# Performance work log

Measured on AMD Instinct MI355X. Metric: run time of the kernel, lower is better.

The kernel has to match this reference:

```python
import jax, jax.numpy as jnp
import numpy as np
from jax import lax

C_IN = 256
C_OUT = 256
KS = 3


def _conv(x, w, b):
    # x: [B,C,H,W], w: [O,I,kh,kw] -> NCHW 'SAME' conv, stride 1
    y = lax.conv_general_dilated(x, w, window_strides=(1, 1), padding='SAME',
                                 dimension_numbers=('NCHW', 'OIHW', 'NCHW'))
    return y + b[None, :, None, None]


def setup_inputs() -> dict:
    key = jax.random.key(0)
    ks = jax.random.split(key, 7)
    B, H, W = 2, 64, 64
    fan = C_IN * KS * KS
    lim = float(np.sqrt(6.0 / (fan + C_OUT * KS * KS)))  # xavier uniform
    return {
        'x': jax.random.normal(ks[0], (B, C_IN, H, W), jnp.float32),
        'ref_x': jax.random.normal(ks[1], (B, C_IN, H, W), jnp.float32),
        'conv1_w': jax.random.uniform(ks[2], (C_OUT, C_IN, KS, KS), jnp.float32, -lim, lim),
        'conv1_b': jnp.zeros((C_OUT,), jnp.float32),
        'conv2_w': jax.random.uniform(ks[3], (C_OUT, C_IN, KS, KS), jnp.float32, -lim, lim),
        'conv2_b': jnp.zeros((C_OUT,), jnp.float32),
        'gamma': jnp.array([0.5], jnp.float32),
    }


def reference(x, ref_x, conv1_w, conv1_b, conv2_w, conv2_b, gamma):
    B, Cin, H, W = x.shape
    HW = H * W
    x_f = jax.nn.relu(_conv(x, conv1_w, conv1_b)).reshape(B, C_OUT, HW)        # [B,C,HW]
    r_f = jax.nn.relu(_conv(ref_x, conv1_w, conv1_b))                          # [B,C,H,W]
    r_f = r_f.transpose(0, 2, 3, 1).reshape(B, HW, C_OUT)                      # [B,HW,C]
    corr = jnp.einsum('bnc,bcm->bnm', r_f, x_f)                                # [B,HW,HW]
    corr = jax.nn.softmax(corr, axis=1)                                        # softmax over ref positions
    ref_c2 = jax.nn.relu(_conv(x, conv2_w, conv2_b)).reshape(B, C_OUT, HW)     # [B,C,HW]
    A = jnp.einsum('bcn,bnm->bcm', ref_c2, corr).reshape(x.shape)              # [B,C,H,W]
    return A * gamma[0] + x
```

## Files before the change

### kernel.cpp

```cpp
#include <hip/hip_runtime.h>
#include <hip/hip_bf16.h>

#define B_ 2
#define C_ 256
#define H_ 64
#define W_ 64
#define N_ 4096

typedef short bf16x8 __attribute__((ext_vector_type(8)));
typedef _Float16 f16x8 __attribute__((ext_vector_type(8)));
typedef float f32x4 __attribute__((ext_vector_type(4)));

static __device__ __forceinline__ unsigned short f2bf(float f) {
    union { float f; unsigned u; } uf; uf.f = f;
    unsigned r = uf.u + 0x7fffu + ((uf.u >> 16) & 1u);
    return (unsigned short)(r >> 16);
}
static __device__ __forceinline__ unsigned short f2h_u(float f) {
    union { _Float16 h; unsigned short u; } c; c.h = (_Float16)f; return c.u;
}

static __device__ __forceinline__ void gload16(const void* g, void* l) {
    __builtin_amdgcn_global_load_lds(
        (const __attribute__((address_space(1))) unsigned int*)g,
        (__attribute__((address_space(3))) unsigned int*)l, 16, 0, 0);
}

__global__ __launch_bounds__(256) void cvt_x_k(const float* __restrict__ x,
                                               const float* __restrict__ ref_x,
                                               unsigned short* __restrict__ xtx,
                                               unsigned short* __restrict__ xtr)
{
    __shared__ unsigned short t[64][72];
    const int pt = blockIdx.x, ct = blockIdx.y;
    const int which = blockIdx.z >> 1, b = blockIdx.z & 1;
    const float* in = which ? ref_x : x;
    unsigned short* out = which ? xtr : xtx;
    const int a = threadIdx.x & 63, r = threadIdx.x >> 6;
    #pragma unroll
    for (int i = 0; i < 16; ++i) {
        int c = i * 4 + r;
        t[c][a] = f2h_u(in[((size_t)(b * C_ + ct * 64 + c) << 12) + pt * 64 + a]);
    }
    __syncthreads();
    #pragma unroll
    for (int i = 0; i < 16; ++i) {
        int p = i * 4 + r;
        out[((size_t)(b * N_ + pt * 64 + p) << 8) + ct * 64 + a] = t[a][p];
    }
}

__global__ __launch_bounds__(256) void cvt_w_k(const float* __restrict__ w1,
                                               const float* __restrict__ w2,
                                               unsigned short* __restrict__ wh1,
                                               unsigned short* __restrict__ wh2)
{
    int g = blockIdx.x;
    const float* w = (g < 2304) ? w1 : w2;
    unsigned short* wh = (g < 2304) ? wh1 : wh2;
    int i = (g % 2304) * 256 + threadIdx.x;
    int ci = i & 255, co = (i >> 8) & 255, tap = i >> 16;
    wh[i] = f2h_u(w[((size_t)(co * 256 + ci)) * 9 + tap]);
}

__global__ __launch_bounds__(256) void conv_mfma_k(
    const unsigned short* __restrict__ xtx, const unsigned short* __restrict__ xtr,
    const unsigned short* __restrict__ w1h, const unsigned short* __restrict__ w2h,
    const float* __restrict__ b1, const float* __restrict__ b2,
    unsigned short* __restrict__ f1x, unsigned short* __restrict__ f1r,
    unsigned short* __restrict__ f2)
{
    __shared__ unsigned short As[4 * 576 * 8];
    __shared__ unsigned short Bs[4 * 66 * 32];
    const int tid = threadIdx.x;
    const int pt  = blockIdx.x;
    const int cot = blockIdx.y;
    const int cid = blockIdx.z >> 1;
    const int b   = blockIdx.z & 1;

    const unsigned short* xt = (cid == 1) ? xtr : xtx;
    const unsigned short* wt = (cid == 2) ? w2h : w1h;
    const float* bias = (cid == 2) ? b2 : b1;
    unsigned short* out = (cid == 0) ? f1x : (cid == 1) ? f1r : f2;
    const int trans = (cid != 2);

    const int lane = tid & 63, wid = tid >> 6;
    const int wco = wid >> 1, wpos = wid & 1;
    const int rl = lane & 15, q = lane >> 4;
    const int r0 = pt * 2;

    f32x4 acc[2][4];
    #pragma unroll
    for (int mi = 0; mi < 2; ++mi)
        #pragma unroll
        for (int ni = 0; ni < 4; ++ni)
            #pragma unroll
            for (int e = 0; e < 4; ++e) acc[mi][ni][e] = 0.f;

    for (int k0 = 0; k0 < C_; k0 += 32) {
        #pragma unroll
        for (int tap = 0; tap < 9; ++tap) {
            gload16(wt + ((size_t)(tap * C_ + cot * 64 + lane) << 8) + k0 + wid * 8,
                    &As[(wid * 576 + tap * 64 + lane) * 8]);
        }
        #pragma unroll
        for (int j = 0; j < 5; ++j) {
            int it = tid + j * 256;
            if (it < 1056) {
                int col = it >> 4, sub = it & 15;
                int row = sub >> 2, qb = sub & 3;
                int h = r0 + row - 1, c = col - 1;
                float4 v; v.x = 0.f; v.y = 0.f; v.z = 0.f; v.w = 0.f;
                if (h >= 0 && h < 64 && c >= 0 && c < 64)
                    v = *(const float4*)(xt + ((size_t)(b * N_ + h * 64 + c) << 8) + k0 + qb * 8);
                int chunk = qb ^ ((col >> 1) & 3);
                *(float4*)&Bs[(row * 66 + col) * 32 + chunk * 8] = v;
            }
        }
        __syncthreads();

        #pragma unroll
        for (int tap = 0; tap < 9; ++tap) {
            const int kh = tap / 3, kw = tap % 3;
            f16x8 a0 = *(const f16x8*)&As[(q * 576 + tap * 64 + wco * 32 + rl) * 8];
            f16x8 a1 = *(const f16x8*)&As[(q * 576 + tap * 64 + wco * 32 + 16 + rl) * 8];
            const int chunkB = q ^ (((rl + kw) >> 1) & 3);
            const int rowB = (wpos + kh) * 66;
            #pragma unroll
            for (int ni = 0; ni < 4; ++ni) {
                int colB = ni * 16 + rl + kw;
                f16x8 bf = *(const f16x8*)&Bs[(rowB + colB) * 32 + chunkB * 8];
                acc[0][ni] = __builtin_amdgcn_mfma_f32_16x16x32_f16(a0, bf, acc[0][ni], 0, 0, 0);
                acc[1][ni] = __builtin_amdgcn_mfma_f32_16x16x32_f16(a1, bf, acc[1][ni], 0, 0, 0);
            }
        }
        __syncthreads();
    }

    #pragma unroll
    for (int mi = 0; mi < 2; ++mi) {
        const int co = cot * 64 + wco * 32 + mi * 16 + q * 4;
        float bs[4];
        #pragma unroll
        for (int rr = 0; rr < 4; ++rr) bs[rr] = bias[co + rr];
        #pragma unroll
        for (int ni = 0; ni < 4; ++ni) {
            const int pos = pt * 128 + wpos * 64 + ni * 16 + rl;
            if (trans) {
                unsigned short pk[4];
                #pragma unroll
                for (int rr = 0; rr < 4; ++rr)
                    pk[rr] = f2bf(fmaxf(acc[mi][ni][rr] + bs[rr], 0.f));
                uint2 u;
                u.x = (unsigned)pk[0] | ((unsigned)pk[1] << 16);
                u.y = (unsigned)pk[2] | ((unsigned)pk[3] << 16);
                *(uint2*)&out[((size_t)(b * N_ + pos) << 8) + co] = u;
            } else {
                #pragma unroll
                for (int rr = 0; rr < 4; ++rr)
                    out[((size_t)(b * C_ + co + rr) << 12) + pos] =
                        f2bf(fmaxf(acc[mi][ni][rr] + bs[rr], 0.f));
            }
        }
    }
}

__global__ __launch_bounds__(256) void gemm_corr_k(
    const unsigned short* __restrict__ f1x, const unsigned short* __restrict__ f1r,
    float* __restrict__ corr)
{
    __shared__ alignas(16) unsigned short As[128 * 32];
    __shared__ alignas(16) unsigned short Bs[128 * 32];
    const int tid = threadIdx.x;
    const int tn = blockIdx.x, tm = blockIdx.y, b = blockIdx.z;

    const unsigned short* Ab = f1x + ((size_t)b * N_ + (size_t)tm * 128) * C_;
    const unsigned short* Bb = f1r + ((size_t)b * N_ + (size_t)tn * 128) * C_;

    const int wid = tid >> 6, lane = tid & 63;
    const int wr = wid >> 1, wc = wid & 1;
    const int rl = lane & 15, q = lane >> 4;
    const int srow = wid * 32 + (lane >> 2), sq = lane & 3;

    f32x4 acc[4][4];
    #pragma unroll
    for (int mi = 0; mi < 4; ++mi)
        #pragma unroll
        for (int ni = 0; ni < 4; ++ni)
            #pragma unroll
            for (int e = 0; e < 4; ++e) acc[mi][ni][e] = 0.f;

    for (int k0 = 0; k0 < C_; k0 += 32) {
        gload16(&Ab[(size_t)srow * C_ + k0 + sq * 8],        &As[srow * 32 + sq * 8]);
        gload16(&Ab[(size_t)(srow + 16) * C_ + k0 + sq * 8], &As[(srow + 16) * 32 + sq * 8]);
        gload16(&Bb[(size_t)srow * C_ + k0 + sq * 8],        &Bs[srow * 32 + sq * 8]);
        gload16(&Bb[(size_t)(srow + 16) * C_ + k0 + sq * 8], &Bs[(srow + 16) * 32 + sq * 8]);
        __syncthreads();
        bf16x8 a[4], bb[4];
        #pragma unroll
        for (int mi = 0; mi < 4; ++mi)
            a[mi] = *(const bf16x8*)&As[(wr * 64 + mi * 16 + rl) * 32 + q * 8];
        #pragma unroll
        for (int ni = 0; ni < 4; ++ni)
            bb[ni] = *(const bf16x8*)&Bs[(wc * 64 + ni * 16 + rl) * 32 + q * 8];
        #pragma unroll
        for (int mi = 0; mi < 4; ++mi)
            #pragma unroll
            for (int ni = 0; ni < 4; ++ni)
                acc[mi][ni] = __builtin_amdgcn_mfma_f32_16x16x32_bf16(a[mi], bb[ni], acc[mi][ni], 0, 0, 0);
        __syncthreads();
    }

    #pragma unroll
    for (int mi = 0; mi < 4; ++mi)
        #pragma unroll
        for (int ni = 0; ni < 4; ++ni)
            #pragma unroll
            for (int rr = 0; rr < 4; ++rr) {
                int m = tm * 128 + wr * 64 + mi * 16 + q * 4 + rr;
                int n = tn * 128 + wc * 64 + ni * 16 + rl;
                corr[((size_t)b * N_ + m) * N_ + n] = acc[mi][ni][rr];
            }
}

__global__ __launch_bounds__(256) void softmax_rows_k(float* __restrict__ corr)
{
    __shared__ float red[4];
    const int m = blockIdx.x, b = blockIdx.y;
    float* row = corr + ((size_t)b * N_ + m) * N_;
    float4* row4 = (float4*)row;
    const int tid = threadIdx.x;
    const int wid = tid >> 6, lane = tid & 63;

    float4 v[4];
    float mx = -3.0e38f;
    #pragma unroll
    for (int j = 0; j < 4; ++j) {
        v[j] = row4[tid + j * 256];
        mx = fmaxf(mx, fmaxf(fmaxf(v[j].x, v[j].y), fmaxf(v[j].z, v[j].w)));
    }
    #pragma unroll
    for (int off = 32; off; off >>= 1) mx = fmaxf(mx, __shfl_xor(mx, off));
    if (lane == 0) red[wid] = mx;
    __syncthreads();
    mx = fmaxf(fmaxf(red[0], red[1]), fmaxf(red[2], red[3]));
    __syncthreads();

    float s = 0.f;
    #pragma unroll
    for (int j = 0; j < 4; ++j) {
        v[j].x = __expf(v[j].x - mx);
        v[j].y = __expf(v[j].y - mx);
        v[j].z = __expf(v[j].z - mx);
        v[j].w = __expf(v[j].w - mx);
        s += v[j].x + v[j].y + v[j].z + v[j].w;
    }
    #pragma unroll
    for (int off = 32; off; off >>= 1) s += __shfl_xor(s, off);
    if (lane == 0) red[wid] = s;
    __syncthreads();
    s = red[0] + red[1] + red[2] + red[3];
    const float inv = 1.f / s;

    unsigned short* rb = (unsigned short*)row;
    #pragma unroll
    for (int j = 0; j < 4; ++j) {
        uint2 u;
        u.x = (unsigned)f2bf(v[j].x * inv) | ((unsigned)f2bf(v[j].y * inv) << 16);
        u.y = (unsigned)f2bf(v[j].z * inv) | ((unsigned)f2bf(v[j].w * inv) << 16);
        *(uint2*)&rb[4 * (tid + j * 256)] = u;
    }
}

__global__ __launch_bounds__(512) void gemm_out_k(
    const unsigned short* __restrict__ f2, float* __restrict__ corr)
{
    __shared__ alignas(16) unsigned short As[128 * 32];
    __shared__ alignas(16) unsigned short Bs[128 * 32];
    const int tid = threadIdx.x;
    const int tm = blockIdx.x;
    const int tc = blockIdx.y >> 2;
    const int s  = blockIdx.y & 3;
    const int b  = blockIdx.z;

    const unsigned short* Ab = f2 + ((size_t)b * C_ + (size_t)tc * 128) * N_;
    const unsigned short* Bb = (const unsigned short*)corr
                             + ((size_t)b * N_ + (size_t)tm * 128) * 8192;

    const int wid = tid >> 6, lane = tid & 63;
    const int wc = wid >> 2, wm = wid & 3;
    const int rl = lane & 15, q = lane >> 4;
    const int srow = wid * 16 + (lane >> 2), sq = lane & 3;
    const int nbase = s * 1024;

    f32x4 acc[4][2];
    #pragma unroll
    for (int mi = 0; mi < 4; ++mi)
        #pragma unroll
        for (int ni = 0; ni < 2; ++ni)
            #pragma unroll
            for (int e = 0; e < 4; ++e) acc[mi][ni][e] = 0.f;

    for (int kk = 0; kk < 32; ++kk) {
        const int k0 = nbase + kk * 32;
        gload16(&Ab[(size_t)srow * N_ + k0 + sq * 8],   &As[srow * 32 + sq * 8]);
        gload16(&Bb[(size_t)srow * 8192 + k0 + sq * 8], &Bs[srow * 32 + sq * 8]);
        __syncthreads();
        bf16x8 a[4], bb[2];
        #pragma unroll
        for (int mi = 0; mi < 4; ++mi)
            a[mi] = *(const bf16x8*)&As[(wc * 64 + mi * 16 + rl) * 32 + q * 8];
        #pragma unroll
        for (int ni = 0; ni < 2; ++ni)
            bb[ni] = *(const bf16x8*)&Bs[(wm * 32 + ni * 16 + rl) * 32 + q * 8];
        #pragma unroll
        for (int mi = 0; mi < 4; ++mi)
            #pragma unroll
            for (int ni = 0; ni < 2; ++ni)
                acc[mi][ni] = __builtin_amdgcn_mfma_f32_16x16x32_bf16(a[mi], bb[ni], acc[mi][ni], 0, 0, 0);
        __syncthreads();
    }

    #pragma unroll
    for (int mi = 0; mi < 4; ++mi)
        #pragma unroll
        for (int ni = 0; ni < 2; ++ni)
            #pragma unroll
            for (int rr = 0; rr < 4; ++rr) {
                int c = tc * 128 + wc * 64 + mi * 16 + q * 4 + rr;
                int m = tm * 128 + wm * 32 + ni * 16 + rl;
                size_t e = (((size_t)(s * 2 + b) * C_ + c) << 12) + m;
                corr[(e >> 11) * 4096 + 2048 + (e & 2047)] = acc[mi][ni][rr];
            }
}

__global__ __launch_bounds__(256) void reduce_k(
    const float* __restrict__ corr, const float* __restrict__ x,
    const float* __restrict__ gamma, float* __restrict__ out)
{
    const float g = gamma[0];
    size_t i = (size_t)blockIdx.x * 256 + threadIdx.x;
    size_t idx = i << 2;
    float4 sum; sum.x = 0.f; sum.y = 0.f; sum.z = 0.f; sum.w = 0.f;
    #pragma unroll
    for (int sp = 0; sp < 4; ++sp) {
        size_t e = (size_t)sp * 2097152 + idx;
        float4 v = *(const float4*)&corr[(e >> 11) * 4096 + 2048 + (e & 2047)];
        sum.x += v.x; sum.y += v.y; sum.z += v.z; sum.w += v.w;
    }
    float4 xv = ((const float4*)x)[i];
    float4 o;
    o.x = sum.x * g + xv.x;
    o.y = sum.y * g + xv.y;
    o.z = sum.z * g + xv.z;
    o.w = sum.w * g + xv.w;
    ((float4*)out)[i] = o;
}

extern "C" void kernel_launch(void* const* d_in, const int* in_sizes, int n_in,
                              void* d_out, int out_size, void* d_ws, size_t ws_size,
                              hipStream_t stream) {
    const float* x     = (const float*)d_in[0];
    const float* ref_x = (const float*)d_in[1];
    const float* w1    = (const float*)d_in[2];
    const float* b1    = (const float*)d_in[3];
    const float* w2    = (const float*)d_in[4];
    const float* b2    = (const float*)d_in[5];
    const float* gamma = (const float*)d_in[6];
    float* out = (float*)d_out;

    char* ws = (char*)d_ws;
    size_t off = 0;
    auto nxt = [&](size_t bytes) {
        char* p = ws + off;
        off += (bytes + 255) & ~(size_t)255;
        return p;
    };
    unsigned short* f1x = (unsigned short*)nxt((size_t)B_ * N_ * C_ * 2);
    unsigned short* f1r = (unsigned short*)nxt((size_t)B_ * N_ * C_ * 2);
    unsigned short* f2  = (unsigned short*)nxt((size_t)B_ * N_ * C_ * 2);
    unsigned short* xtx = (unsigned short*)nxt((size_t)B_ * N_ * C_ * 2);
    unsigned short* xtr = (unsigned short*)nxt((size_t)B_ * N_ * C_ * 2);
    unsigned short* w1h = (unsigned short*)nxt((size_t)9 * C_ * C_ * 2);
    unsigned short* w2h = (unsigned short*)nxt((size_t)9 * C_ * C_ * 2);
    float* corr = (float*)nxt((size_t)B_ * N_ * N_ * 4);

    cvt_x_k<<<dim3(64, 4, 4), 256, 0, stream>>>(x, ref_x, xtx, xtr);
    cvt_w_k<<<4608, 256, 0, stream>>>(w1, w2, w1h, w2h);

    conv_mfma_k<<<dim3(32, 4, 6), 256, 0, stream>>>(xtx, xtr, w1h, w2h, b1, b2,
                                                    f1x, f1r, f2);

    gemm_corr_k<<<dim3(32, 32, B_), 256, 0, stream>>>(f1x, f1r, corr);
    softmax_rows_k<<<dim3(N_, B_), 256, 0, stream>>>(corr);
    gemm_out_k<<<dim3(32, 8, B_), 512, 0, stream>>>(f2, corr);
    reduce_k<<<2048, 256, 0, stream>>>(corr, x, gamma, out);
}
```

Measured before the change: 162.3 us.

## Switch conv and correlation GEMMs to 32x32x16 MFMA with larger conv tiles

```diff
diff --git a/kernel.cpp b/kernel.cpp
--- a/kernel.cpp
+++ b/kernel.cpp
@@ -10,6 +10,7 @@
 typedef short bf16x8 __attribute__((ext_vector_type(8)));
 typedef _Float16 f16x8 __attribute__((ext_vector_type(8)));
 typedef float f32x4 __attribute__((ext_vector_type(4)));
+typedef float f32x16 __attribute__((ext_vector_type(16)));
 
 static __device__ __forceinline__ unsigned short f2bf(float f) {
     union { float f; unsigned u; } uf; uf.f = f;
@@ -70,8 +71,8 @@
     unsigned short* __restrict__ f1x, unsigned short* __restrict__ f1r,
     unsigned short* __restrict__ f2)
 {
-    __shared__ unsigned short As[4 * 576 * 8];
-    __shared__ unsigned short Bs[4 * 66 * 32];
+    __shared__ unsigned short As[9 * 64 * 32];
+    __shared__ unsigned short Bs[6 * 66 * 32];
     const int tid = threadIdx.x;
     const int pt  = blockIdx.x;
     const int cot = blockIdx.y;
@@ -85,30 +86,31 @@
     const int trans = (cid != 2);
 
     const int lane = tid & 63, wid = tid >> 6;
-    const int wco = wid >> 1, wpos = wid & 1;
-    const int rl = lane & 15, q = lane >> 4;
-    const int r0 = pt * 2;
-
-    f32x4 acc[2][4];
-    #pragma unroll
-    for (int mi = 0; mi < 2; ++mi)
-        #pragma unroll
-        for (int ni = 0; ni < 4; ++ni)
-            #pragma unroll
-            for (int e = 0; e < 4; ++e) acc[mi][ni][e] = 0.f;
+    const int rl32 = lane & 31, l5 = lane >> 5;
+    const int r0 = pt * 4;
+
+    f32x16 acc[2][2];
+    #pragma unroll
+    for (int fm = 0; fm < 2; ++fm)
+        #pragma unroll
+        for (int fn = 0; fn < 2; ++fn)
+            #pragma unroll
+            for (int e = 0; e < 16; ++e) acc[fm][fn][e] = 0.f;
 
     for (int k0 = 0; k0 < C_; k0 += 32) {
         #pragma unroll
         for (int tap = 0; tap < 9; ++tap) {
-            gload16(wt + ((size_t)(tap * C_ + cot * 64 + lane) << 8) + k0 + wid * 8,
-                    &As[(wid * 576 + tap * 64 + lane) * 8]);
+            gload16(wt + ((size_t)(tap * C_ + cot * 64 + wid * 16 + (lane >> 2)) << 8)
+                       + k0 + (lane & 3) * 8,
+                    &As[tap * 2048 + wid * 512 + lane * 8]);
         }
         #pragma unroll
-        for (int j = 0; j < 5; ++j) {
+        for (int j = 0; j < 7; ++j) {
             int it = tid + j * 256;
-            if (it < 1056) {
-                int col = it >> 4, sub = it & 15;
-                int row = sub >> 2, qb = sub & 3;
+            if (it < 1584) {
+                int col = it / 24;
+                int rem = it - col * 24;
+                int row = rem >> 2, qb = rem & 3;
                 int h = r0 + row - 1, c = col - 1;
                 float4 v; v.x = 0.f; v.y = 0.f; v.z = 0.f; v.w = 0.f;
                 if (h >= 0 && h < 64 && c >= 0 && c < 64)
@@ -122,47 +124,60 @@
         #pragma unroll
         for (int tap = 0; tap < 9; ++tap) {
             const int kh = tap / 3, kw = tap % 3;
-            f16x8 a0 = *(const f16x8*)&As[(q * 576 + tap * 64 + wco * 32 + rl) * 8];
-            f16x8 a1 = *(const f16x8*)&As[(q * 576 + tap * 64 + wco * 32 + 16 + rl) * 8];
-            const int chunkB = q ^ (((rl + kw) >> 1) & 3);
-            const int rowB = (wpos + kh) * 66;
-            #pragma unroll
-            for (int ni = 0; ni < 4; ++ni) {
-                int colB = ni * 16 + rl + kw;
-                f16x8 bf = *(const f16x8*)&Bs[(rowB + colB) * 32 + chunkB * 8];
-                acc[0][ni] = __builtin_amdgcn_mfma_f32_16x16x32_f16(a0, bf, acc[0][ni], 0, 0, 0);
-                acc[1][ni] = __builtin_amdgcn_mfma_f32_16x16x32_f16(a1, bf, acc[1][ni], 0, 0, 0);
+            f16x8 a[2][2], bb[2][2];
+            #pragma unroll
+            for (int fm = 0; fm < 2; ++fm)
+                #pragma unroll
+                for (int kk = 0; kk < 2; ++kk)
+                    a[fm][kk] = *(const f16x8*)&As[(tap * 64 + fm * 32 + rl32) * 32 + kk * 16 + l5 * 8];
+            #pragma unroll
+            for (int fn = 0; fn < 2; ++fn) {
+                const int colB = fn * 32 + rl32 + kw;
+                const int sw = ((rl32 + kw) >> 1) & 3;
+                #pragma unroll
+                for (int kk = 0; kk < 2; ++kk) {
+                    const int kc = kk * 2 + l5;
+                    bb[fn][kk] = *(const f16x8*)&Bs[((wid + kh) * 66 + colB) * 32 + (kc ^ sw) * 8];
+                }
+            }
+            #pragma unroll
+            for (int fm = 0; fm < 2; ++fm)
+                #pragma unroll
+                for (int fn = 0; fn < 2; ++fn)
+                    #pragma unroll
+                    for (int kk = 0; kk < 2; ++kk)
+                        acc[fm][fn] = __builtin_amdgcn_mfma_f32_32x32x16_f16(
+                            a[fm][kk], bb[fn][kk], acc[fm][fn], 0, 0, 0);
+        }
+        __syncthreads();
+    }
+
+    const int prow = r0 + wid;
+    #pragma unroll
+    for (int fm = 0; fm < 2; ++fm)
+        #pragma unroll
+        for (int fn = 0; fn < 2; ++fn) {
+            const int pos = prow * 64 + fn * 32 + rl32;
+            #pragma unroll
+            for (int g = 0; g < 4; ++g) {
+                const int co0 = cot * 64 + fm * 32 + g * 8 + l5 * 4;
+                if (trans) {
+                    unsigned short pk[4];
+                    #pragma unroll
+                    for (int rr = 0; rr < 4; ++rr)
+                        pk[rr] = f2bf(fmaxf(acc[fm][fn][g * 4 + rr] + bias[co0 + rr], 0.f));
+                    uint2 u;
+                    u.x = (unsigned)pk[0] | ((unsigned)pk[1] << 16);
+                    u.y = (unsigned)pk[2] | ((unsigned)pk[3] << 16);
+                    *(uint2*)&out[((size_t)(b * N_ + pos) << 8) + co0] = u;
+                } else {
+                    #pragma unroll
+                    for (int rr = 0; rr < 4; ++rr)
+                        out[((size_t)(b * C_ + co0 + rr) << 12) + pos] =
+                            f2bf(fmaxf(acc[fm][fn][g * 4 + rr] + bias[co0 + rr], 0.f));
+                }
             }
         }
-        __syncthreads();
-    }
-
-    #pragma unroll
-    for (int mi = 0; mi < 2; ++mi) {
-        const int co = cot * 64 + wco * 32 + mi * 16 + q * 4;
-        float bs[4];
-        #pragma unroll
-        for (int rr = 0; rr < 4; ++rr) bs[rr] = bias[co + rr];
-        #pragma unroll
-        for (int ni = 0; ni < 4; ++ni) {
-            const int pos = pt * 128 + wpos * 64 + ni * 16 + rl;
-            if (trans) {
-                unsigned short pk[4];
-                #pragma unroll
-                for (int rr = 0; rr < 4; ++rr)
-                    pk[rr] = f2bf(fmaxf(acc[mi][ni][rr] + bs[rr], 0.f));
-                uint2 u;
-                u.x = (unsigned)pk[0] | ((unsigned)pk[1] << 16);
-                u.y = (unsigned)pk[2] | ((unsigned)pk[3] << 16);
-                *(uint2*)&out[((size_t)(b * N_ + pos) << 8) + co] = u;
-            } else {
-                #pragma unroll
-                for (int rr = 0; rr < 4; ++rr)
-                    out[((size_t)(b * C_ + co + rr) << 12) + pos] =
-                        f2bf(fmaxf(acc[mi][ni][rr] + bs[rr], 0.f));
-            }
-        }
-    }
 }
 
 __global__ __launch_bounds__(256) void gemm_corr_k(
@@ -179,16 +194,16 @@
 
     const int wid = tid >> 6, lane = tid & 63;
     const int wr = wid >> 1, wc = wid & 1;
-    const int rl = lane & 15, q = lane >> 4;
+    const int rl32 = lane & 31, l5 = lane >> 5;
     const int srow = wid * 32 + (lane >> 2), sq = lane & 3;
 
-    f32x4 acc[4][4];
-    #pragma unroll
-    for (int mi = 0; mi < 4; ++mi)
-        #pragma unroll
-        for (int ni = 0; ni < 4; ++ni)
-            #pragma unroll
-            for (int e = 0; e < 4; ++e) acc[mi][ni][e] = 0.f;
+    f32x16 acc[2][2];
+    #pragma unroll
+    for (int fm = 0; fm < 2; ++fm)
+        #pragma unroll
+        for (int fn = 0; fn < 2; ++fn)
+            #pragma unroll
+            for (int e = 0; e < 16; ++e) acc[fm][fn][e] = 0.f;
 
     for (int k0 = 0; k0 < C_; k0 += 32) {
         gload16(&Ab[(size_t)srow * C_ + k0 + sq * 8],        &As[srow * 32 + sq * 8]);
@@ -196,31 +211,41 @@
         gload16(&Bb[(size_t)srow * C_ + k0 + sq * 8],        &Bs[srow * 32 + sq * 8]);
         gload16(&Bb[(size_t)(srow + 16) * C_ + k0 + sq * 8], &Bs[(srow + 16) * 32 + sq * 8]);
         __syncthreads();
-        bf16x8 a[4], bb[4];
-        #pragma unroll
-        for (int mi = 0; mi < 4; ++mi)
-            a[mi] = *(const bf16x8*)&As[(wr * 64 + mi * 16 + rl) * 32 + q * 8];
-        #pragma unroll
-        for (int ni = 0; ni < 4; ++ni)
-            bb[ni] = *(const bf16x8*)&Bs[(wc * 64 + ni * 16 + rl) * 32 + q * 8];
-        #pragma unroll
-        for (int mi = 0; mi < 4; ++mi)
-            #pragma unroll
-            for (int ni = 0; ni < 4; ++ni)
-                acc[mi][ni] = __builtin_amdgcn_mfma_f32_16x16x32_bf16(a[mi], bb[ni], acc[mi][ni], 0, 0, 0);
-        __syncthreads();
-    }
-
-    #pragma unroll
-    for (int mi = 0; mi < 4; ++mi)
-        #pragma unroll
-        for (int ni = 0; ni < 4; ++ni)
-            #pragma unroll
-            for (int rr = 0; rr < 4; ++rr) {
-                int m = tm * 128 + wr * 64 + mi * 16 + q * 4 + rr;
-                int n = tn * 128 + wc * 64 + ni * 16 + rl;
-                corr[((size_t)b * N_ + m) * N_ + n] = acc[mi][ni][rr];
+        bf16x8 a[2][2], bb[2][2];
+        #pragma unroll
+        for (int fm = 0; fm < 2; ++fm)
+            #pragma unroll
+            for (int kk = 0; kk < 2; ++kk)
+                a[fm][kk] = *(const bf16x8*)&As[(wr * 64 + fm * 32 + rl32) * 32 + kk * 16 + l5 * 8];
+        #pragma unroll
+        for (int fn = 0; fn < 2; ++fn)
+            #pragma unroll
+            for (int kk = 0; kk < 2; ++kk)
+                bb[fn][kk] = *(const bf16x8*)&Bs[(wc * 64 + fn * 32 + rl32) * 32 + kk * 16 + l5 * 8];
+        #pragma unroll
+        for (int fm = 0; fm < 2; ++fm)
+            #pragma unroll
+            for (int fn = 0; fn < 2; ++fn)
+                #pragma unroll
+                for (int kk = 0; kk < 2; ++kk)
+                    acc[fm][fn] = __builtin_amdgcn_mfma_f32_32x32x16_bf16(
+                        a[fm][kk], bb[fn][kk], acc[fm][fn], 0, 0, 0);
+        __syncthreads();
+    }
+
+    #pragma unroll
+    for (int fm = 0; fm < 2; ++fm)
+        #pragma unroll
+        for (int fn = 0; fn < 2; ++fn) {
+            const int n = tn * 128 + wc * 64 + fn * 32 + rl32;
+            #pragma unroll
+            for (int g = 0; g < 4; ++g) {
+                const int m0 = tm * 128 + wr * 64 + fm * 32 + g * 8 + l5 * 4;
+                #pragma unroll
+                for (int rr = 0; rr < 4; ++rr)
+                    corr[((size_t)b * N_ + m0 + rr) * N_ + n] = acc[fm][fn][g * 4 + rr];
             }
+        }
 }
 
 __global__ __launch_bounds__(256) void softmax_rows_k(float* __restrict__ corr)
@@ -388,7 +413,7 @@
     cvt_x_k<<<dim3(64, 4, 4), 256, 0, stream>>>(x, ref_x, xtx, xtr);
     cvt_w_k<<<4608, 256, 0, stream>>>(w1, w2, w1h, w2h);
 
-    conv_mfma_k<<<dim3(32, 4, 6), 256, 0, stream>>>(xtx, xtr, w1h, w2h, b1, b2,
+    conv_mfma_k<<<dim3(16, 4, 6), 256, 0, stream>>>(xtx, xtr, w1h, w2h, b1, b2,
                                                     f1x, f1r, f2);
 
     gemm_corr_k<<<dim3(32, 32, B_), 256, 0, stream>>>(f1x, f1r, corr);
```

Result: no change. 163.6 us (+0.8%).

## Restructure conv to 2-wave blocks with direct weight loads; swizzle GEMM LDS tiles

Applied to the files above, without the earlier changes.

```diff
diff --git a/kernel.cpp b/kernel.cpp
--- a/kernel.cpp
+++ b/kernel.cpp
@@ -63,14 +63,13 @@
     wh[i] = f2h_u(w[((size_t)(co * 256 + ci)) * 9 + tap]);
 }
 
-__global__ __launch_bounds__(256) void conv_mfma_k(
+__global__ __launch_bounds__(128) void conv_mfma_k(
     const unsigned short* __restrict__ xtx, const unsigned short* __restrict__ xtr,
     const unsigned short* __restrict__ w1h, const unsigned short* __restrict__ w2h,
     const float* __restrict__ b1, const float* __restrict__ b2,
     unsigned short* __restrict__ f1x, unsigned short* __restrict__ f1r,
     unsigned short* __restrict__ f2)
 {
-    __shared__ unsigned short As[4 * 576 * 8];
     __shared__ unsigned short Bs[4 * 66 * 32];
     const int tid = threadIdx.x;
     const int pt  = blockIdx.x;
@@ -85,27 +84,21 @@
     const int trans = (cid != 2);
 
     const int lane = tid & 63, wid = tid >> 6;
-    const int wco = wid >> 1, wpos = wid & 1;
     const int rl = lane & 15, q = lane >> 4;
     const int r0 = pt * 2;
 
-    f32x4 acc[2][4];
-    #pragma unroll
-    for (int mi = 0; mi < 2; ++mi)
-        #pragma unroll
-        for (int ni = 0; ni < 4; ++ni)
-            #pragma unroll
-            for (int e = 0; e < 4; ++e) acc[mi][ni][e] = 0.f;
+    f32x4 acc[4][4];
+    #pragma unroll
+    for (int cf = 0; cf < 4; ++cf)
+        #pragma unroll
+        for (int pf = 0; pf < 4; ++pf)
+            #pragma unroll
+            for (int e = 0; e < 4; ++e) acc[cf][pf][e] = 0.f;
 
     for (int k0 = 0; k0 < C_; k0 += 32) {
         #pragma unroll
-        for (int tap = 0; tap < 9; ++tap) {
-            gload16(wt + ((size_t)(tap * C_ + cot * 64 + lane) << 8) + k0 + wid * 8,
-                    &As[(wid * 576 + tap * 64 + lane) * 8]);
-        }
-        #pragma unroll
-        for (int j = 0; j < 5; ++j) {
-            int it = tid + j * 256;
+        for (int j = 0; j < 9; ++j) {
+            int it = tid + j * 128;
             if (it < 1056) {
                 int col = it >> 4, sub = it & 15;
                 int row = sub >> 2, qb = sub & 3;
@@ -122,44 +115,49 @@
         #pragma unroll
         for (int tap = 0; tap < 9; ++tap) {
             const int kh = tap / 3, kw = tap % 3;
-            f16x8 a0 = *(const f16x8*)&As[(q * 576 + tap * 64 + wco * 32 + rl) * 8];
-            f16x8 a1 = *(const f16x8*)&As[(q * 576 + tap * 64 + wco * 32 + 16 + rl) * 8];
-            const int chunkB = q ^ (((rl + kw) >> 1) & 3);
-            const int rowB = (wpos + kh) * 66;
-            #pragma unroll
-            for (int ni = 0; ni < 4; ++ni) {
-                int colB = ni * 16 + rl + kw;
-                f16x8 bf = *(const f16x8*)&Bs[(rowB + colB) * 32 + chunkB * 8];
-                acc[0][ni] = __builtin_amdgcn_mfma_f32_16x16x32_f16(a0, bf, acc[0][ni], 0, 0, 0);
-                acc[1][ni] = __builtin_amdgcn_mfma_f32_16x16x32_f16(a1, bf, acc[1][ni], 0, 0, 0);
+            f16x8 w[4];
+            #pragma unroll
+            for (int cf = 0; cf < 4; ++cf)
+                w[cf] = *(const f16x8*)&wt[((size_t)(tap * C_ + cot * 64 + cf * 16 + rl) << 8)
+                                           + k0 + q * 8];
+            const int rowB = (wid + kh) * 66;
+            const int swz = ((rl + kw) >> 1) & 3;
+            #pragma unroll
+            for (int pf = 0; pf < 4; ++pf) {
+                const int colB = pf * 16 + rl + kw;
+                f16x8 xv = *(const f16x8*)&Bs[(rowB + colB) * 32 + (q ^ swz) * 8];
+                #pragma unroll
+                for (int cf = 0; cf < 4; ++cf)
+                    acc[cf][pf] = __builtin_amdgcn_mfma_f32_16x16x32_f16(w[cf], xv, acc[cf][pf], 0, 0, 0);
             }
         }
         __syncthreads();
     }
 
-    #pragma unroll
-    for (int mi = 0; mi < 2; ++mi) {
-        const int co = cot * 64 + wco * 32 + mi * 16 + q * 4;
+    const int prow = r0 + wid;
+    #pragma unroll
+    for (int cf = 0; cf < 4; ++cf) {
+        const int co0 = cot * 64 + cf * 16 + q * 4;
         float bs[4];
         #pragma unroll
-        for (int rr = 0; rr < 4; ++rr) bs[rr] = bias[co + rr];
-        #pragma unroll
-        for (int ni = 0; ni < 4; ++ni) {
-            const int pos = pt * 128 + wpos * 64 + ni * 16 + rl;
+        for (int rr = 0; rr < 4; ++rr) bs[rr] = bias[co0 + rr];
+        #pragma unroll
+        for (int pf = 0; pf < 4; ++pf) {
+            const int pos = prow * 64 + pf * 16 + rl;
             if (trans) {
                 unsigned short pk[4];
                 #pragma unroll
                 for (int rr = 0; rr < 4; ++rr)
-                    pk[rr] = f2bf(fmaxf(acc[mi][ni][rr] + bs[rr], 0.f));
+                    pk[rr] = f2bf(fmaxf(acc[cf][pf][rr] + bs[rr], 0.f));
                 uint2 u;
                 u.x = (unsigned)pk[0] | ((unsigned)pk[1] << 16);
                 u.y = (unsigned)pk[2] | ((unsigned)pk[3] << 16);
-                *(uint2*)&out[((size_t)(b * N_ + pos) << 8) + co] = u;
+                *(uint2*)&out[((size_t)(b * N_ + pos) << 8) + co0] = u;
             } else {
                 #pragma unroll
                 for (int rr = 0; rr < 4; ++rr)
-                    out[((size_t)(b * C_ + co + rr) << 12) + pos] =
-                        f2bf(fmaxf(acc[mi][ni][rr] + bs[rr], 0.f));
+                    out[((size_t)(b * C_ + co0 + rr) << 12) + pos] =
+                        f2bf(fmaxf(acc[cf][pf][rr] + bs[rr], 0.f));
             }
         }
     }
@@ -181,6 +179,8 @@
     const int wr = wid >> 1, wc = wid & 1;
     const int rl = lane & 15, q = lane >> 4;
     const int srow = wid * 32 + (lane >> 2), sq = lane & 3;
+    const int logq = sq ^ ((lane >> 3) & 3);
+    const int rswz = (rl >> 1) & 3;
 
     f32x4 acc[4][4];
     #pragma unroll
@@ -191,18 +191,18 @@
             for (int e = 0; e < 4; ++e) acc[mi][ni][e] = 0.f;
 
     for (int k0 = 0; k0 < C_; k0 += 32) {
-        gload16(&Ab[(size_t)srow * C_ + k0 + sq * 8],        &As[srow * 32 + sq * 8]);
-        gload16(&Ab[(size_t)(srow + 16) * C_ + k0 + sq * 8], &As[(srow + 16) * 32 + sq * 8]);
-        gload16(&Bb[(size_t)srow * C_ + k0 + sq * 8],        &Bs[srow * 32 + sq * 8]);
-        gload16(&Bb[(size_t)(srow + 16) * C_ + k0 + sq * 8], &Bs[(srow + 16) * 32 + sq * 8]);
+        gload16(&Ab[(size_t)srow * C_ + k0 + logq * 8],        &As[srow * 32 + sq * 8]);
+        gload16(&Ab[(size_t)(srow + 16) * C_ + k0 + logq * 8], &As[(srow + 16) * 32 + sq * 8]);
+        gload16(&Bb[(size_t)srow * C_ + k0 + logq * 8],        &Bs[srow * 32 + sq * 8]);
+        gload16(&Bb[(size_t)(srow + 16) * C_ + k0 + logq * 8], &Bs[(srow + 16) * 32 + sq * 8]);
         __syncthreads();
         bf16x8 a[4], bb[4];
         #pragma unroll
         for (int mi = 0; mi < 4; ++mi)
-            a[mi] = *(const bf16x8*)&As[(wr * 64 + mi * 16 + rl) * 32 + q * 8];
+            a[mi] = *(const bf16x8*)&As[(wr * 64 + mi * 16 + rl) * 32 + (q ^ rswz) * 8];
         #pragma unroll
         for (int ni = 0; ni < 4; ++ni)
-            bb[ni] = *(const bf16x8*)&Bs[(wc * 64 + ni * 16 + rl) * 32 + q * 8];
+            bb[ni] = *(const bf16x8*)&Bs[(wc * 64 + ni * 16 + rl) * 32 + (q ^ rswz) * 8];
         #pragma unroll
         for (int mi = 0; mi < 4; ++mi)
             #pragma unroll
@@ -291,6 +291,8 @@
     const int wc = wid >> 2, wm = wid & 3;
     const int rl = lane & 15, q = lane >> 4;
     const int srow = wid * 16 + (lane >> 2), sq = lane & 3;
+    const int logq = sq ^ ((lane >> 3) & 3);
+    const int rswz = (rl >> 1) & 3;
     const int nbase = s * 1024;
 
     f32x4 acc[4][2];
@@ -303,16 +305,16 @@
 
     for (int kk = 0; kk < 32; ++kk) {
         const int k0 = nbase + kk * 32;
-        gload16(&Ab[(size_t)srow * N_ + k0 + sq * 8],   &As[srow * 32 + sq * 8]);
-        gload16(&Bb[(size_t)srow * 8192 + k0 + sq * 8], &Bs[srow * 32 + sq * 8]);
+        gload16(&Ab[(size_t)srow * N_ + k0 + logq * 8],   &As[srow * 32 + sq * 8]);
+        gload16(&Bb[(size_t)srow * 8192 + k0 + logq * 8], &Bs[srow * 32 + sq * 8]);
         __syncthreads();
         bf16x8 a[4], bb[2];
         #pragma unroll
         for (int mi = 0; mi < 4; ++mi)
-            a[mi] = *(const bf16x8*)&As[(wc * 64 + mi * 16 + rl) * 32 + q * 8];
+            a[mi] = *(const bf16x8*)&As[(wc * 64 + mi * 16 + rl) * 32 + (q ^ rswz) * 8];
         #pragma unroll
         for (int ni = 0; ni < 2; ++ni)
-            bb[ni] = *(const bf16x8*)&Bs[(wm * 32 + ni * 16 + rl) * 32 + q * 8];
+            bb[ni] = *(const bf16x8*)&Bs[(wm * 32 + ni * 16 + rl) * 32 + (q ^ rswz) * 8];
         #pragma unroll
         for (int mi = 0; mi < 4; ++mi)
             #pragma unroll
@@ -388,7 +390,7 @@
     cvt_x_k<<<dim3(64, 4, 4), 256, 0, stream>>>(x, ref_x, xtx, xtr);
     cvt_w_k<<<4608, 256, 0, stream>>>(w1, w2, w1h, w2h);
 
-    conv_mfma_k<<<dim3(32, 4, 6), 256, 0, stream>>>(xtx, xtr, w1h, w2h, b1, b2,
+    conv_mfma_k<<<dim3(32, 4, 6), 128, 0, stream>>>(xtx, xtr, w1h, w2h, b1, b2,
                                                     f1x, f1r, f2);
 
     gemm_corr_k<<<dim3(32, 32, B_), 256, 0, stream>>>(f1x, f1r, corr);
```

After: 180.5 us. 11.2% more time.

## Swizzle LDS layout and remap workgroup order in correlation and output GEMMs

Applied to the files above, without the earlier changes.

```diff
diff --git a/kernel.cpp b/kernel.cpp
--- a/kernel.cpp
+++ b/kernel.cpp
@@ -172,7 +172,10 @@
     __shared__ alignas(16) unsigned short As[128 * 32];
     __shared__ alignas(16) unsigned short Bs[128 * 32];
     const int tid = threadIdx.x;
-    const int tn = blockIdx.x, tm = blockIdx.y, b = blockIdx.z;
+    const int wg  = blockIdx.x + (blockIdx.y << 5);
+    const int swz = (wg & 7) * 128 + (wg >> 3);
+    const int tn = swz & 31, tm = swz >> 5;
+    const int b  = blockIdx.z;
 
     const unsigned short* Ab = f1x + ((size_t)b * N_ + (size_t)tm * 128) * C_;
     const unsigned short* Bb = f1r + ((size_t)b * N_ + (size_t)tn * 128) * C_;
@@ -181,6 +184,8 @@
     const int wr = wid >> 1, wc = wid & 1;
     const int rl = lane & 15, q = lane >> 4;
     const int srow = wid * 32 + (lane >> 2), sq = lane & 3;
+    const int logq = sq ^ ((lane >> 3) & 3);
+    const int rswz = (rl >> 1) & 3;
 
     f32x4 acc[4][4];
     #pragma unroll
@@ -191,18 +196,18 @@
             for (int e = 0; e < 4; ++e) acc[mi][ni][e] = 0.f;
 
     for (int k0 = 0; k0 < C_; k0 += 32) {
-        gload16(&Ab[(size_t)srow * C_ + k0 + sq * 8],        &As[srow * 32 + sq * 8]);
-        gload16(&Ab[(size_t)(srow + 16) * C_ + k0 + sq * 8], &As[(srow + 16) * 32 + sq * 8]);
-        gload16(&Bb[(size_t)srow * C_ + k0 + sq * 8],        &Bs[srow * 32 + sq * 8]);
-        gload16(&Bb[(size_t)(srow + 16) * C_ + k0 + sq * 8], &Bs[(srow + 16) * 32 + sq * 8]);
+        gload16(&Ab[(size_t)srow * C_ + k0 + logq * 8],        &As[srow * 32 + sq * 8]);
+        gload16(&Ab[(size_t)(srow + 16) * C_ + k0 + logq * 8], &As[(srow + 16) * 32 + sq * 8]);
+        gload16(&Bb[(size_t)srow * C_ + k0 + logq * 8],        &Bs[srow * 32 + sq * 8]);
+        gload16(&Bb[(size_t)(srow + 16) * C_ + k0 + logq * 8], &Bs[(srow + 16) * 32 + sq * 8]);
         __syncthreads();
         bf16x8 a[4], bb[4];
         #pragma unroll
         for (int mi = 0; mi < 4; ++mi)
-            a[mi] = *(const bf16x8*)&As[(wr * 64 + mi * 16 + rl) * 32 + q * 8];
+            a[mi] = *(const bf16x8*)&As[(wr * 64 + mi * 16 + rl) * 32 + (q ^ rswz) * 8];
         #pragma unroll
         for (int ni = 0; ni < 4; ++ni)
-            bb[ni] = *(const bf16x8*)&Bs[(wc * 64 + ni * 16 + rl) * 32 + q * 8];
+            bb[ni] = *(const bf16x8*)&Bs[(wc * 64 + ni * 16 + rl) * 32 + (q ^ rswz) * 8];
         #pragma unroll
         for (int mi = 0; mi < 4; ++mi)
             #pragma unroll
@@ -278,9 +283,11 @@
     __shared__ alignas(16) unsigned short As[128 * 32];
     __shared__ alignas(16) unsigned short Bs[128 * 32];
     const int tid = threadIdx.x;
-    const int tm = blockIdx.x;
-    const int tc = blockIdx.y >> 2;
-    const int s  = blockIdx.y & 3;
+    const int wg  = blockIdx.x + (blockIdx.y << 5);
+    const int swz = (wg & 7) * 32 + (wg >> 3);
+    const int tm = swz & 31;
+    const int tc = (swz >> 5) >> 2;
+    const int s  = (swz >> 5) & 3;
     const int b  = blockIdx.z;
 
     const unsigned short* Ab = f2 + ((size_t)b * C_ + (size_t)tc * 128) * N_;
@@ -291,6 +298,8 @@
     const int wc = wid >> 2, wm = wid & 3;
     const int rl = lane & 15, q = lane >> 4;
     const int srow = wid * 16 + (lane >> 2), sq = lane & 3;
+    const int logq = sq ^ ((lane >> 3) & 3);
+    const int rswz = (rl >> 1) & 3;
     const int nbase = s * 1024;
 
     f32x4 acc[4][2];
@@ -303,16 +312,16 @@
 
     for (int kk = 0; kk < 32; ++kk) {
         const int k0 = nbase + kk * 32;
-        gload16(&Ab[(size_t)srow * N_ + k0 + sq * 8],   &As[srow * 32 + sq * 8]);
-        gload16(&Bb[(size_t)srow * 8192 + k0 + sq * 8], &Bs[srow * 32 + sq * 8]);
+        gload16(&Ab[(size_t)srow * N_ + k0 + logq * 8],   &As[srow * 32 + sq * 8]);
+        gload16(&Bb[(size_t)srow * 8192 + k0 + logq * 8], &Bs[srow * 32 + sq * 8]);
         __syncthreads();
         bf16x8 a[4], bb[2];
         #pragma unroll
         for (int mi = 0; mi < 4; ++mi)
-            a[mi] = *(const bf16x8*)&As[(wc * 64 + mi * 16 + rl) * 32 + q * 8];
+            a[mi] = *(const bf16x8*)&As[(wc * 64 + mi * 16 + rl) * 32 + (q ^ rswz) * 8];
         #pragma unroll
         for (int ni = 0; ni < 2; ++ni)
-            bb[ni] = *(const bf16x8*)&Bs[(wm * 32 + ni * 16 + rl) * 32 + q * 8];
+            bb[ni] = *(const bf16x8*)&Bs[(wm * 32 + ni * 16 + rl) * 32 + (q ^ rswz) * 8];
         #pragma unroll
         for (int mi = 0; mi < 4; ++mi)
             #pragma unroll
```

After: 176.4 us. 1.09x slower.
